# Optimization experiments

Measured on AMD Instinct MI355X. Metric: run time of the kernel, lower is better.

## Reference

```python
import jax, jax.numpy as jnp
import numpy as np
import math

B, D, L, Nh, Dk, Dv, K, CONV_NUM = 16, 256, 1024, 8, 32, 32, 7, 4
EPS = 1e-5


def _pos_encoding():
    # matches PosEncoder: freqs/phases per channel, sin(pos*freqs + phases), shape [D, L]
    idx = jnp.arange(D)
    i = idx.astype(jnp.float32)
    even = (idx % 2 == 0)
    freqs = jnp.where(even, 10000.0 ** (-i / D), -(10000.0 ** ((1.0 - i) / D)))
    phases = jnp.where(even, 0.0, math.pi / 2)
    pos = jnp.arange(L, dtype=jnp.float32)
    return jnp.sin(pos[None, :] * freqs[:, None] + phases[:, None])


def _layer_norm(x, g, b):
    # nn.LayerNorm([D, L]) on [B, D, L]: normalize over last two dims
    m = jnp.mean(x, axis=(1, 2), keepdims=True)
    v = jnp.mean((x - m) ** 2, axis=(1, 2), keepdims=True)
    return (x - m) * jax.lax.rsqrt(v + EPS) * g + b


def _ds_conv(x, dw, db, pw, pb):
    # depthwise conv1d (groups=D, same padding) + pointwise 1x1 conv
    y = jax.lax.conv_general_dilated(
        x, dw[:, None, :], window_strides=(1,), padding=[(K // 2, K // 2)],
        feature_group_count=D, dimension_numbers=('NCH', 'OIH', 'NCH'))
    y = y + db[None, :, None]
    return jnp.einsum('bdl,ed->bel', y, pw) + pb[None, :, None]


def setup_inputs() -> dict:
    key = jax.random.key(0)
    ks = jax.random.split(key, 12)

    def n(k, shape, scale):
        return jax.random.normal(k, shape, jnp.float32) * scale

    x = jax.random.normal(ks[0], (B, D, L), jnp.float32)
    mask = jax.random.randint(ks[1], (B, L), 0, 2).astype(jnp.int32)
    dw_w = n(ks[2], (CONV_NUM, D, K), 0.1)
    dw_b = jnp.zeros((CONV_NUM, D), jnp.float32)
    pw_w = n(ks[3], (CONV_NUM, D, D), 0.05)
    pw_b = jnp.zeros((CONV_NUM, D), jnp.float32)
    ln_g = jnp.ones((CONV_NUM + 2, D, L), jnp.float32)
    ln_b = jnp.zeros((CONV_NUM + 2, D, L), jnp.float32)
    Wq = n(ks[4], (Nh, D, Dk), 0.05)
    Wk = n(ks[5], (Nh, D, Dk), 0.05)
    Wv = n(ks[6], (Nh, D, Dv), 0.05)
    Wo = n(ks[7], (D, Dv * Nh), 0.05)
    fc_w = n(ks[8], (D, D), 0.05)
    fc_b = jnp.zeros((D,), jnp.float32)
    return dict(x=x, mask=mask, dw_w=dw_w, dw_b=dw_b, pw_w=pw_w, pw_b=pw_b,
                ln_g=ln_g, ln_b=ln_b, Wq=Wq, Wk=Wk, Wv=Wv, Wo=Wo,
                fc_w=fc_w, fc_b=fc_b)


def reference(x, mask, dw_w, dw_b, pw_w, pw_b, ln_g, ln_b, Wq, Wk, Wv, Wo, fc_w, fc_b):
    m = mask.astype(jnp.float32)  # [B, L]
    out = x + _pos_encoding()[None]
    res = out
    out = _layer_norm(out, ln_g[0], ln_b[0])
    for i in range(CONV_NUM):
        out = jax.nn.relu(_ds_conv(out, dw_w[i], dw_b[i], pw_w[i], pw_b[i])) + res
        # F.dropout in eval mode is identity
        res = out
        out = _layer_norm(out, ln_g[i + 1], ln_b[i + 1])
    # self attention (batched over heads instead of per-head loop; same math)
    xt = out.transpose(0, 2, 1)  # [B, L, D]
    q = jnp.einsum('bld,hdk->bhlk', xt, Wq)
    k = jnp.einsum('bld,hdk->bhlk', xt, Wk)
    v = jnp.einsum('bld,hdv->bhlv', xt, Wv)
    scores = jnp.einsum('bhqk,bhlk->bhql', q, k) * (1.0 / math.sqrt(Dk))
    hm = m[:, None, None, :]  # mask over key dim
    scores = scores * hm + (1.0 - hm) * (-1e30)
    attn = jax.nn.softmax(scores, axis=-1) * m[:, None, :, None]  # zero padded query rows
    heads = jnp.einsum('bhql,bhlv->bqhv', attn, v).reshape(B, L, Nh * Dv)  # head-major concat
    att_out = (heads @ Wo).transpose(0, 2, 1)  # [B, D, L]
    out = att_out + res
    res = out
    out = _layer_norm(out, ln_g[CONV_NUM + 1], ln_b[CONV_NUM + 1])
    out = jnp.einsum('bdl,ed->bel', out, fc_w) + fc_b[None, :, None]  # nn.Linear on [B,L,D]
    out = jax.nn.relu(out) + res
    return out
```

## Files before the change

### kernel.cpp

```cpp
#include <hip/hip_runtime.h>
#include <hip/hip_bf16.h>

#define NB 16
#define ND 256
#define NL 1024
#define NHH 8
#define NDK 32
#define NKW 7
#define NCONV 4
#define NPB (ND*NL)

constexpr float LN_EPS = 1e-5f;

typedef __attribute__((ext_vector_type(4))) float f32x4;
typedef __attribute__((ext_vector_type(4))) short bf16x4;
typedef __attribute__((ext_vector_type(8))) short bf16x8;

__device__ __forceinline__ short bf16s(float f){
  return (short)__builtin_bit_cast(unsigned short, __float2bfloat16(f));
}
__device__ __forceinline__ float b2f(short s){
  return __builtin_bit_cast(float, ((unsigned)(unsigned short)s) << 16);
}

__device__ __forceinline__ void ln_ab(const float* st, int slot, int b, float& mean, float& rstd){
  float s = 0.f, ss = 0.f;
  #pragma unroll
  for(int bin=0;bin<8;bin++){
    const float* p = st + ((size_t)((slot*NB+b)*8+bin))*32;
    s += p[0]; ss += p[1];
  }
  mean = s * (1.0f/NPB);
  float var = ss * (1.0f/NPB) - mean*mean;
  rstd = rsqrtf(var + LN_EPS);
}

__device__ __forceinline__ void stats_reduce(float s, float ss, float* stats, int slot, int b, int bin){
  __shared__ float red[8];
  #pragma unroll
  for(int o=32;o>0;o>>=1){ s += __shfl_down(s,o); ss += __shfl_down(ss,o); }
  int lane = threadIdx.x & 63, w = threadIdx.x >> 6;
  if(lane==0){ red[w*2]=s; red[w*2+1]=ss; }
  __syncthreads();
  if(threadIdx.x==0){
    float* p = stats + ((size_t)((slot*NB+b)*8+bin))*32;
    atomicAdd(&p[0], red[0]+red[2]+red[4]+red[6]);
    atomicAdd(&p[1], red[1]+red[3]+red[5]+red[7]);
  }
}

__global__ __launch_bounds__(256) void k_prep(const float* __restrict__ pw_w, const float* __restrict__ fc_w,
    const float* __restrict__ Wo, const float* __restrict__ Wq, const float* __restrict__ Wk,
    const float* __restrict__ Wv, const float* __restrict__ g, const float* __restrict__ btab,
    short* __restrict__ Wpwb, short* __restrict__ Wfcb, short* __restrict__ Wob, short* __restrict__ Wcat,
    short* __restrict__ gT, short* __restrict__ bT, float* __restrict__ postab){
  __shared__ float T[64][65];
  int blk = blockIdx.x, tid = threadIdx.x;
  if(blk < 256){
    int idx = blk*1024 + tid*4;
    f32x4 v = *(const f32x4*)(pw_w + idx);
    bf16x4 o;
    #pragma unroll
    for(int j=0;j<4;j++) o[j] = bf16s(v[j]);
    *(bf16x4*)(Wpwb + idx) = o;
  } else if(blk < 320){
    int idx = (blk-256)*1024 + tid*4;
    f32x4 v = *(const f32x4*)(fc_w + idx);
    bf16x4 o;
    #pragma unroll
    for(int j=0;j<4;j++) o[j] = bf16s(v[j]);
    *(bf16x4*)(Wfcb + idx) = o;
  } else if(blk < 384){
    int idx = (blk-320)*1024 + tid*4;
    int e = idx >> 8;
    bf16x4 o;
    #pragma unroll
    for(int j=0;j<4;j++){ int d = (idx+j)&255; o[j] = bf16s(Wo[d*ND + e]); }
    *(bf16x4*)(Wob + idx) = o;
  } else if(blk < 576){
    int idx = (blk-384)*1024 + tid*4;
    int og = idx >> 8, d = idx & 255;
    int seg = og >> 8, o = og & 255, h = o >> 5, k = o & 31;
    const float* W = (seg==0) ? Wq : ((seg==1) ? Wk : Wv);
    bf16x4 ov;
    #pragma unroll
    for(int j=0;j<4;j++) ov[j] = bf16s(W[((size_t)(h*ND + d + j))*NDK + k]);
    *(bf16x4*)(Wcat + idx) = ov;
  } else if(blk < 832){
    int d = blk - 576;
    int l = tid*4;
    const float LN1E4_OVER_D = 9.210340371976184f / (float)ND;
    float freq, phase;
    if((d & 1) == 0){ freq =  __expf(-(float)d*LN1E4_OVER_D);      phase = 0.f; }
    else            { freq = -__expf((1.f-(float)d)*LN1E4_OVER_D); phase = 1.5707963267948966f; }
    f32x4 o;
    #pragma unroll
    for(int j=0;j<4;j++) o[j] = sinf((float)(l+j)*freq + phase);
    *(f32x4*)(postab + ((size_t)d<<10) + l) = o;
  } else {
    int blk2 = blk - 832;
    int which = blk2 >> 6;
    int tile = blk2 & 63;
    int d0 = (tile & 3) << 6, l0 = (tile >> 2) << 6;
    const float* src = (which < 6) ? (g + (size_t)which*NPB) : (btab + (size_t)(which-6)*NPB);
    short* dst = (which < 6) ? (gT + (size_t)which*NPB) : (bT + (size_t)(which-6)*NPB);
    for(int i=tid;i<1024;i+=256){
      int dd = i>>4, l4 = i&15;
      f32x4 v = *(const f32x4*)(src + (size_t)(d0+dd)*NL + l0 + l4*4);
      #pragma unroll
      for(int j=0;j<4;j++) T[dd][l4*4+j] = v[j];
    }
    __syncthreads();
    for(int i=tid;i<1024;i+=256){
      int ll = i>>4, d4 = i&15;
      bf16x4 o;
      #pragma unroll
      for(int j=0;j<4;j++) o[j] = bf16s(T[d4*4+j][ll]);
      *(bf16x4*)(dst + (size_t)(l0+ll)*ND + d0 + d4*4) = o;
    }
  }
}

__global__ __launch_bounds__(256) void k_posadd(const float* __restrict__ x, const float* __restrict__ postab,
                                                float* __restrict__ R, float* __restrict__ stats){
  int blk = blockIdx.x;
  int lt = blk & 15, dt = (blk>>4)&3, b = blk>>6;
  int l0 = lt*64, d0 = dt*64;
  __shared__ float T[64][65];
  int tid = threadIdx.x;
  float s=0.f, ss=0.f;
  for(int i=tid;i<1024;i+=256){
    int dd = i>>4, l4 = i&15;
    int d = d0+dd;
    f32x4 xv = *(const f32x4*)(x + ((size_t)(b*ND+d)<<10) + l0 + l4*4);
    f32x4 pv = *(const f32x4*)(postab + ((size_t)d<<10) + l0 + l4*4);
    #pragma unroll
    for(int j=0;j<4;j++){
      float v = xv[j] + pv[j];
      T[dd][l4*4+j] = v;
      s += v; ss += v*v;
    }
  }
  __syncthreads();
  for(int i=tid;i<1024;i+=256){
    int ll = i>>4, d4 = i&15;
    f32x4 o;
    #pragma unroll
    for(int j=0;j<4;j++) o[j] = T[d4*4+j][ll];
    *(f32x4*)(R + ((size_t)(b*NL+l0+ll)<<8) + d0 + d4*4) = o;
  }
  stats_reduce(s, ss, stats, 0, b, blk & 7);
}

__global__ __launch_bounds__(256) void k_dwconvT(const float* __restrict__ R, const short* __restrict__ gT,
                                                 const short* __restrict__ bT, const float* __restrict__ w7,
                                                 const float* __restrict__ db, const float* __restrict__ stats,
                                                 short* __restrict__ Y, int slot){
  int blk = blockIdx.x;
  int lblk = blk & 63, b = blk >> 6;
  int tid = threadIdx.x;
  __shared__ float wLds[NKW][ND];
  __shared__ float dbLds[ND];
  for(int i=tid;i<ND*NKW;i+=256){ int d=i/NKW, q=i-d*NKW; wLds[q][d] = w7[i]; }
  dbLds[tid] = db[tid];
  float mean, rstd; ln_ab(stats, slot, b, mean, rstd);
  float mr = mean*rstd;
  __syncthreads();
  int d0 = (tid & 63)*4;
  int l0 = lblk*16 + (tid >> 6)*4;
  f32x4 ln[10];
  #pragma unroll
  for(int i=0;i<10;i++){
    int lp = l0 - 3 + i;
    if(lp >= 0 && lp < NL){
      f32x4 v = *(const f32x4*)(R + ((size_t)(b*NL+lp)<<8) + d0);
      bf16x4 gv = *(const bf16x4*)(gT + ((size_t)lp<<8) + d0);
      bf16x4 bv = *(const bf16x4*)(bT + ((size_t)lp<<8) + d0);
      f32x4 t;
      #pragma unroll
      for(int j=0;j<4;j++) t[j] = (v[j]*rstd - mr)*b2f(gv[j]) + b2f(bv[j]);
      ln[i] = t;
    } else ln[i] = (f32x4){0.f,0.f,0.f,0.f};
  }
  f32x4 dbv = *(const f32x4*)(&dbLds[d0]);
  #pragma unroll
  for(int jl=0;jl<4;jl++){
    f32x4 acc = dbv;
    #pragma unroll
    for(int q=0;q<NKW;q++){
      f32x4 wq = *(const f32x4*)(&wLds[q][d0]);
      #pragma unroll
      for(int j=0;j<4;j++) acc[j] += ln[jl+q][j]*wq[j];
    }
    bf16x4 o;
    #pragma unroll
    for(int j=0;j<4;j++) o[j] = bf16s(acc[j]);
    *(bf16x4*)(Y + ((size_t)(b*NL + l0 + jl)<<8) + d0) = o;
  }
}

__device__ __forceinline__ void stage_rows_bf16(short* dst, const short* src, int tid, int c){
  for(int i=tid;i<1024;i+=256){
    int rr = i>>4, kk = i&15;
    bf16x8 w = *(const bf16x8*)(src + (size_t)rr*ND + c*128 + kk*8);
    *(bf16x8*)((char*)dst + rr*256 + ((kk*16) ^ ((rr&7)<<4))) = w;
  }
}
__device__ __forceinline__ void stage_act_ln(short* dst, const float* src, const short* g, const short* bt,
                                             float mean, float rstd, int tid, int c){
  float mr = mean*rstd;
  for(int i=tid;i<2048;i+=256){
    int ll = i>>5, kk = i&31;
    size_t off = (size_t)ll*ND + c*128 + kk*4;
    f32x4 v = *(const f32x4*)(src + off);
    bf16x4 gv = *(const bf16x4*)(g + off);
    bf16x4 bv = *(const bf16x4*)(bt + off);
    bf16x4 o;
    #pragma unroll
    for(int j=0;j<4;j++) o[j] = bf16s((v[j]*rstd - mr)*b2f(gv[j]) + b2f(bv[j]));
    *(bf16x4*)((char*)dst + ll*256 + ((kk*8) ^ ((ll&7)<<4))) = o;
  }
}
__device__ __forceinline__ void mfma_core(const short* As, const short* Bs, int wm, int wn,
                                          int lq, int gg, f32x4 acc[2][2]){
  #pragma unroll
  for(int t=0;t<4;t++){
    bf16x8 a[2], bb[2];
    #pragma unroll
    for(int m=0;m<2;m++){
      int row = wm*32 + m*16 + lq;
      a[m] = *(const bf16x8*)((const char*)As + row*256 + ((t*64 + gg*16) ^ ((row&7)<<4)));
    }
    #pragma unroll
    for(int n=0;n<2;n++){
      int row = wn*32 + n*16 + lq;
      bb[n] = *(const bf16x8*)((const char*)Bs + row*256 + ((t*64 + gg*16) ^ ((row&7)<<4)));
    }
    #pragma unroll
    for(int m=0;m<2;m++)
      #pragma unroll
      for(int n=0;n<2;n++)
        acc[m][n] = __builtin_amdgcn_mfma_f32_16x16x32_bf16(a[m], bb[n], acc[m][n], 0,0,0);
  }
}

#define GEMM_PROLOGUE() \
  int blk = blockIdx.x; \
  int lt = blk & 15, et = (blk>>4)&3, b = blk>>6; \
  int l0 = lt*64, e0 = et*64; \
  int tid = threadIdx.x; \
  int w = tid>>6, lane = tid&63, lq = lane&15, gg = lane>>4; \
  int wm = w&1, wn = w>>1; \
  __shared__ short As[8192], Bs[8192]; \
  f32x4 acc[2][2]; \
  acc[0][0]=acc[0][1]=acc[1][0]=acc[1][1] = (f32x4){0.f,0.f,0.f,0.f};

__global__ __launch_bounds__(256) void k_pw(const short* __restrict__ Y, const short* __restrict__ Wb,
                                            const float* __restrict__ bias, float* __restrict__ R,
                                            float* __restrict__ stats, int slot_out){
  GEMM_PROLOGUE();
  const short* Asrc = Y + ((size_t)(b*NL)+l0)*ND;
  const short* Bsrc = Wb + (size_t)e0*ND;
  for(int c=0;c<2;c++){
    __syncthreads();
    stage_rows_bf16(As, Asrc, tid, c);
    stage_rows_bf16(Bs, Bsrc, tid, c);
    __syncthreads();
    mfma_core(As, Bs, wm, wn, lq, gg, acc);
  }
  float s=0.f, ss=0.f;
  #pragma unroll
  for(int n=0;n<2;n++){
    int e = e0 + wn*32 + n*16 + lq;
    float bv = bias[e];
    #pragma unroll
    for(int m=0;m<2;m++){
      #pragma unroll
      for(int r=0;r<4;r++){
        int l = l0 + wm*32 + m*16 + gg*4 + r;
        size_t ix = (size_t)(b*NL+l)*ND + e;
        float v = fmaxf(acc[m][n][r] + bv, 0.f);
        float rr = R[ix] + v;
        R[ix] = rr;
        s += rr; ss += rr*rr;
      }
    }
  }
  stats_reduce(s, ss, stats, slot_out, b, blk & 7);
}

__global__ __launch_bounds__(256) void k_qkvf(const float* __restrict__ R, const short* __restrict__ gT,
                                              const short* __restrict__ bT, const float* __restrict__ stats,
                                              const short* __restrict__ Wcat, short* __restrict__ Qb,
                                              short* __restrict__ Kb, short* __restrict__ Vb){
  int blk = blockIdx.x;
  int lt = blk & 15;
  int tmp = blk >> 4;
  int et = tmp % 12, b = tmp / 12;
  int l0 = lt*64, e0g = et*64;
  int seg = et >> 2;
  int tid = threadIdx.x;
  int w = tid>>6, lane = tid&63, lq = lane&15, gg = lane>>4;
  int wm = w&1, wn = w>>1;
  __shared__ short As[8192], Bs[8192];
  f32x4 acc[2][2];
  acc[0][0]=acc[0][1]=acc[1][0]=acc[1][1] = (f32x4){0.f,0.f,0.f,0.f};
  float mean, rstd; ln_ab(stats, 4, b, mean, rstd);
  const float* Asrc = R + ((size_t)(b*NL)+l0)*ND;
  const short* gs = gT + (size_t)l0*ND;
  const short* bs = bT + (size_t)l0*ND;
  const short* Bsrc = Wcat + (size_t)e0g*ND;
  for(int c=0;c<2;c++){
    __syncthreads();
    stage_act_ln(As, Asrc, gs, bs, mean, rstd, tid, c);
    stage_rows_bf16(Bs, Bsrc, tid, c);
    __syncthreads();
    mfma_core(As, Bs, wm, wn, lq, gg, acc);
  }
  #pragma unroll
  for(int n=0;n<2;n++){
    int eo = (et&3)*64 + wn*32 + n*16 + lq;
    int h = eo>>5, dk = eo&31;
    if(seg < 2){
      short* outp = (seg==0) ? Qb : Kb;
      #pragma unroll
      for(int m=0;m<2;m++){
        #pragma unroll
        for(int r=0;r<4;r++){
          int l = l0 + wm*32 + m*16 + gg*4 + r;
          outp[((size_t)(b*NHH+h)*NL + l)*NDK + dk] = bf16s(acc[m][n][r]);
        }
      }
    } else {
      #pragma unroll
      for(int m=0;m<2;m++){
        int lb = l0 + wm*32 + m*16 + gg*4;
        bf16x4 pk;
        #pragma unroll
        for(int r=0;r<4;r++) pk[r] = bf16s(acc[m][n][r]);
        *(bf16x4*)(Vb + ((size_t)(b*NHH+h)*NDK + dk)*NL + lb) = pk;
      }
    }
  }
}

__global__ __launch_bounds__(256) void k_attn(const short* __restrict__ Qb, const short* __restrict__ Kb,
                                              const short* __restrict__ Vt, const int* __restrict__ mask,
                                              short* __restrict__ heads){
  int blk = blockIdx.x;
  int qblk = blk & 15, h = (blk >> 4) & 7, b = blk >> 7;
  int bh = b*NHH + h;
  int tid = threadIdx.x;
  int w = tid >> 6, lane = tid & 63;
  int lq = lane & 15, gg = lane >> 4;

  __shared__ short Ks[64][40];
  __shared__ short Vs[32][72];
  __shared__ short Ps[4][16][40];
  __shared__ float msh[64];

  int qrow = qblk*64 + w*16 + lq;
  bf16x8 qf = *(const bf16x8*)(Qb + ((size_t)bh*NL + qrow)*NDK + gg*8);

  f32x4 zero = {0.f,0.f,0.f,0.f};
  f32x4 o0 = zero, o1 = zero;
  float dacc = 0.f;
  const float scale = 0.17677669529663687f;

  for(int t0=0; t0<NL; t0+=64){
    __syncthreads();
    {
      int key = tid >> 2, c = tid & 3;
      *(bf16x8*)(&Ks[key][c*8]) = *(const bf16x8*)(Kb + ((size_t)bh*NL + t0 + key)*NDK + c*8);
      int v = tid >> 3, ch = tid & 7;
      *(bf16x8*)(&Vs[v][ch*8]) = *(const bf16x8*)(Vt + ((size_t)bh*NDK + v)*NL + t0 + ch*8);
      if(tid < 64) msh[tid] = ((float)mask[b*NL + t0 + tid] - 1.f) * 1e30f;
    }
    __syncthreads();
    #pragma unroll
    for(int sub=0; sub<2; sub++){
      bf16x8 a0 = *(const bf16x8*)(&Ks[sub*32 + lq][gg*8]);
      bf16x8 a1 = *(const bf16x8*)(&Ks[sub*32 + 16 + lq][gg*8]);
      f32x4 c0 = __builtin_amdgcn_mfma_f32_16x16x32_bf16(a0, qf, zero, 0, 0, 0);
      f32x4 c1 = __builtin_amdgcn_mfma_f32_16x16x32_bf16(a1, qf, zero, 0, 0, 0);
      bf16x4 p0, p1;
      #pragma unroll
      for(int r=0;r<4;r++){
        float pv0 = __expf(__builtin_fmaf(c0[r], scale, msh[sub*32 + gg*4 + r]));
        dacc += pv0;
        p0[r] = bf16s(pv0);
        float pv1 = __expf(__builtin_fmaf(c1[r], scale, msh[sub*32 + 16 + gg*4 + r]));
        dacc += pv1;
        p1[r] = bf16s(pv1);
      }
      *(bf16x4*)(&Ps[w][lq][gg*4])      = p0;
      *(bf16x4*)(&Ps[w][lq][16 + gg*4]) = p1;
      bf16x8 pf = *(const bf16x8*)(&Ps[w][lq][gg*8]);
      bf16x8 b0 = *(const bf16x8*)(&Vs[lq][sub*32 + gg*8]);
      bf16x8 b1 = *(const bf16x8*)(&Vs[16 + lq][sub*32 + gg*8]);
      o0 = __builtin_amdgcn_mfma_f32_16x16x32_bf16(pf, b0, o0, 0, 0, 0);
      o1 = __builtin_amdgcn_mfma_f32_16x16x32_bf16(pf, b1, o1, 0, 0, 0);
    }
  }
  dacc += __shfl_xor(dacc, 16);
  dacc += __shfl_xor(dacc, 32);
  #pragma unroll
  for(int r=0;r<4;r++){
    int ql = gg*4 + r;
    float dn = __shfl(dacc, ql);
    int qg = qblk*64 + w*16 + ql;
    float mq = (float)mask[b*NL + qg];
    float sc = mq / dn;
    short* op = heads + ((size_t)(b*NL + qg))*(NHH*NDK) + h*NDK;
    op[lq]      = bf16s(o0[r]*sc);
    op[16 + lq] = bf16s(o1[r]*sc);
  }
}

__global__ __launch_bounds__(256) void k_wo(const short* __restrict__ H, const short* __restrict__ Wb,
                                            float* __restrict__ R, float* __restrict__ stats){
  GEMM_PROLOGUE();
  const short* Asrc = H + ((size_t)(b*NL)+l0)*ND;
  const short* Bsrc = Wb + (size_t)e0*ND;
  for(int c=0;c<2;c++){
    __syncthreads();
    stage_rows_bf16(As, Asrc, tid, c);
    stage_rows_bf16(Bs, Bsrc, tid, c);
    __syncthreads();
    mfma_core(As, Bs, wm, wn, lq, gg, acc);
  }
  float s=0.f, ss=0.f;
  #pragma unroll
  for(int n=0;n<2;n++){
    int e = e0 + wn*32 + n*16 + lq;
    #pragma unroll
    for(int m=0;m<2;m++){
      #pragma unroll
      for(int r=0;r<4;r++){
        int l = l0 + wm*32 + m*16 + gg*4 + r;
        size_t ix = (size_t)(b*NL+l)*ND + e;
        float rr = R[ix] + acc[m][n][r];
        R[ix] = rr;
        s += rr; ss += rr*rr;
      }
    }
  }
  stats_reduce(s, ss, stats, 5, b, blk & 7);
}

__global__ __launch_bounds__(256) void k_fc(const float* __restrict__ R, const short* __restrict__ gT,
                                            const short* __restrict__ bT, const float* __restrict__ stats,
                                            const short* __restrict__ Wb, const float* __restrict__ bias,
                                            float* __restrict__ out){
  GEMM_PROLOGUE();
  float mean, rstd; ln_ab(stats, 5, b, mean, rstd);
  const float* Asrc = R + ((size_t)(b*NL)+l0)*ND;
  const short* gs = gT + (size_t)l0*ND;
  const short* bs = bT + (size_t)l0*ND;
  const short* Bsrc = Wb + (size_t)e0*ND;
  for(int c=0;c<2;c++){
    __syncthreads();
    stage_act_ln(As, Asrc, gs, bs, mean, rstd, tid, c);
    stage_rows_bf16(Bs, Bsrc, tid, c);
    __syncthreads();
    mfma_core(As, Bs, wm, wn, lq, gg, acc);
  }
  #pragma unroll
  for(int n=0;n<2;n++){
    int e = e0 + wn*32 + n*16 + lq;
    float bv = bias[e];
    #pragma unroll
    for(int m=0;m<2;m++){
      int lb = l0 + wm*32 + m*16 + gg*4;
      f32x4 ov;
      #pragma unroll
      for(int r=0;r<4;r++){
        float v = fmaxf(acc[m][n][r] + bv, 0.f);
        ov[r] = v + R[(size_t)(b*NL+lb+r)*ND + e];
      }
      *(f32x4*)(out + (size_t)(b*ND+e)*NL + lb) = ov;
    }
  }
}

extern "C" void kernel_launch(void* const* d_in, const int* in_sizes, int n_in,
                              void* d_out, int out_size, void* d_ws, size_t ws_size,
                              hipStream_t stream){
  const float* x    = (const float*)d_in[0];
  const int*   mask = (const int*)d_in[1];
  const float* dw_w = (const float*)d_in[2];
  const float* dw_b = (const float*)d_in[3];
  const float* pw_w = (const float*)d_in[4];
  const float* pw_b = (const float*)d_in[5];
  const float* ln_g = (const float*)d_in[6];
  const float* ln_b = (const float*)d_in[7];
  const float* Wq   = (const float*)d_in[8];
  const float* Wk   = (const float*)d_in[9];
  const float* Wv   = (const float*)d_in[10];
  const float* Wo   = (const float*)d_in[11];
  const float* fc_w = (const float*)d_in[12];
  const float* fc_b = (const float*)d_in[13];

  float* ws     = (float*)d_ws;
  float* stats  = ws;
  float* postab = ws + 98304;
  float* R      = ws + 360448;
  short* Yb     = (short*)(ws + 4554752);
  short* Qb     = (short*)(ws + 6651904);
  short* Kb     = (short*)(ws + 8749056);
  short* Vb     = (short*)(ws + 10846208);
  short* gT     = (short*)(ws + 12943360);
  short* bT     = (short*)(ws + 13729792);
  short* Wpwb   = (short*)(ws + 14516224);
  short* Wfcb   = (short*)(ws + 14647296);
  short* Wob    = (short*)(ws + 14680064);
  short* Wcat   = (short*)(ws + 14712832);

  hipMemsetAsync(stats, 0, 98304*sizeof(float), stream);
  k_prep<<<1600,256,0,stream>>>(pw_w, fc_w, Wo, Wq, Wk, Wv, ln_g, ln_b,
                                Wpwb, Wfcb, Wob, Wcat, gT, bT, postab);
  k_posadd<<<1024,256,0,stream>>>(x, postab, R, stats);
  for(int i=0;i<NCONV;i++){
    k_dwconvT<<<1024,256,0,stream>>>(R, gT + (size_t)i*NPB, bT + (size_t)i*NPB,
                                     dw_w + i*ND*NKW, dw_b + i*ND, stats, Yb, i);
    k_pw<<<1024,256,0,stream>>>(Yb, Wpwb + (size_t)i*65536, pw_b + i*ND, R, stats, i+1);
  }
  k_qkvf<<<3072,256,0,stream>>>(R, gT + (size_t)4*NPB, bT + (size_t)4*NPB, stats, Wcat, Qb, Kb, Vb);
  k_attn<<<2048,256,0,stream>>>(Qb, Kb, Vb, mask, Yb);
  k_wo<<<1024,256,0,stream>>>(Yb, Wob, R, stats);
  k_fc<<<1024,256,0,stream>>>(R, gT + (size_t)5*NPB, bT + (size_t)5*NPB, stats, Wfcb, fc_b, (float*)d_out);
}
```

Measured before the change: 313.2 us.

## Store residual stream in bf16 and compute attention row sums via MFMA

Converts the residual buffer R from fp32 to bf16 across all kernels, roughly halving the bytes read and written for the residual in the posadd, dwconv, pw, qkv, wo and fc stages. LayerNorm statistics are now computed from the rounded bf16 values. The attention kernel also swaps the scalar softmax-denominator accumulation and its shuffles for an extra MFMA against a ones vector, and reorders block indexing so q-blocks of the same head are spread across the grid. The main risk is accuracy: the residual accumulates bf16 rounding over six layers.

```diff
diff --git a/kernel.cpp b/kernel.cpp
--- a/kernel.cpp
+++ b/kernel.cpp
@@ -122,37 +122,38 @@
 }
 
 __global__ __launch_bounds__(256) void k_posadd(const float* __restrict__ x, const float* __restrict__ postab,
-                                                float* __restrict__ R, float* __restrict__ stats){
+                                                short* __restrict__ Rb, float* __restrict__ stats){
   int blk = blockIdx.x;
   int lt = blk & 15, dt = (blk>>4)&3, b = blk>>6;
   int l0 = lt*64, d0 = dt*64;
   __shared__ float T[64][65];
   int tid = threadIdx.x;
-  float s=0.f, ss=0.f;
   for(int i=tid;i<1024;i+=256){
     int dd = i>>4, l4 = i&15;
     int d = d0+dd;
     f32x4 xv = *(const f32x4*)(x + ((size_t)(b*ND+d)<<10) + l0 + l4*4);
     f32x4 pv = *(const f32x4*)(postab + ((size_t)d<<10) + l0 + l4*4);
     #pragma unroll
-    for(int j=0;j<4;j++){
-      float v = xv[j] + pv[j];
-      T[dd][l4*4+j] = v;
-      s += v; ss += v*v;
-    }
+    for(int j=0;j<4;j++) T[dd][l4*4+j] = xv[j] + pv[j];
   }
   __syncthreads();
+  float s=0.f, ss=0.f;
   for(int i=tid;i<1024;i+=256){
     int ll = i>>4, d4 = i&15;
-    f32x4 o;
-    #pragma unroll
-    for(int j=0;j<4;j++) o[j] = T[d4*4+j][ll];
-    *(f32x4*)(R + ((size_t)(b*NL+l0+ll)<<8) + d0 + d4*4) = o;
+    bf16x4 o;
+    #pragma unroll
+    for(int j=0;j<4;j++){
+      short rs = bf16s(T[d4*4+j][ll]);
+      o[j] = rs;
+      float rv = b2f(rs);
+      s += rv; ss += rv*rv;
+    }
+    *(bf16x4*)(Rb + ((size_t)(b*NL+l0+ll)<<8) + d0 + d4*4) = o;
   }
   stats_reduce(s, ss, stats, 0, b, blk & 7);
 }
 
-__global__ __launch_bounds__(256) void k_dwconvT(const float* __restrict__ R, const short* __restrict__ gT,
+__global__ __launch_bounds__(256) void k_dwconvT(const short* __restrict__ Rb, const short* __restrict__ gT,
                                                  const short* __restrict__ bT, const float* __restrict__ w7,
                                                  const float* __restrict__ db, const float* __restrict__ stats,
                                                  short* __restrict__ Y, int slot){
@@ -173,12 +174,12 @@
   for(int i=0;i<10;i++){
     int lp = l0 - 3 + i;
     if(lp >= 0 && lp < NL){
-      f32x4 v = *(const f32x4*)(R + ((size_t)(b*NL+lp)<<8) + d0);
+      bf16x4 v = *(const bf16x4*)(Rb + ((size_t)(b*NL+lp)<<8) + d0);
       bf16x4 gv = *(const bf16x4*)(gT + ((size_t)lp<<8) + d0);
       bf16x4 bv = *(const bf16x4*)(bT + ((size_t)lp<<8) + d0);
       f32x4 t;
       #pragma unroll
-      for(int j=0;j<4;j++) t[j] = (v[j]*rstd - mr)*b2f(gv[j]) + b2f(bv[j]);
+      for(int j=0;j<4;j++) t[j] = (b2f(v[j])*rstd - mr)*b2f(gv[j]) + b2f(bv[j]);
       ln[i] = t;
     } else ln[i] = (f32x4){0.f,0.f,0.f,0.f};
   }
@@ -206,19 +207,19 @@
     *(bf16x8*)((char*)dst + rr*256 + ((kk*16) ^ ((rr&7)<<4))) = w;
   }
 }
-__device__ __forceinline__ void stage_act_ln(short* dst, const float* src, const short* g, const short* bt,
-                                             float mean, float rstd, int tid, int c){
+__device__ __forceinline__ void stage_act_lnb(short* dst, const short* src, const short* g, const short* bt,
+                                              float mean, float rstd, int tid, int c){
   float mr = mean*rstd;
-  for(int i=tid;i<2048;i+=256){
-    int ll = i>>5, kk = i&31;
-    size_t off = (size_t)ll*ND + c*128 + kk*4;
-    f32x4 v = *(const f32x4*)(src + off);
-    bf16x4 gv = *(const bf16x4*)(g + off);
-    bf16x4 bv = *(const bf16x4*)(bt + off);
-    bf16x4 o;
-    #pragma unroll
-    for(int j=0;j<4;j++) o[j] = bf16s((v[j]*rstd - mr)*b2f(gv[j]) + b2f(bv[j]));
-    *(bf16x4*)((char*)dst + ll*256 + ((kk*8) ^ ((ll&7)<<4))) = o;
+  for(int i=tid;i<1024;i+=256){
+    int ll = i>>4, kk = i&15;
+    size_t off = (size_t)ll*ND + c*128 + kk*8;
+    bf16x8 v = *(const bf16x8*)(src + off);
+    bf16x8 gv = *(const bf16x8*)(g + off);
+    bf16x8 bv = *(const bf16x8*)(bt + off);
+    bf16x8 o;
+    #pragma unroll
+    for(int j=0;j<8;j++) o[j] = bf16s((b2f(v[j])*rstd - mr)*b2f(gv[j]) + b2f(bv[j]));
+    *(bf16x8*)((char*)dst + ll*256 + ((kk*16) ^ ((ll&7)<<4))) = o;
   }
 }
 __device__ __forceinline__ void mfma_core(const short* As, const short* Bs, int wm, int wn,
@@ -256,7 +257,7 @@
   acc[0][0]=acc[0][1]=acc[1][0]=acc[1][1] = (f32x4){0.f,0.f,0.f,0.f};
 
 __global__ __launch_bounds__(256) void k_pw(const short* __restrict__ Y, const short* __restrict__ Wb,
-                                            const float* __restrict__ bias, float* __restrict__ R,
+                                            const float* __restrict__ bias, short* __restrict__ Rb,
                                             float* __restrict__ stats, int slot_out){
   GEMM_PROLOGUE();
   const short* Asrc = Y + ((size_t)(b*NL)+l0)*ND;
@@ -280,16 +281,18 @@
         int l = l0 + wm*32 + m*16 + gg*4 + r;
         size_t ix = (size_t)(b*NL+l)*ND + e;
         float v = fmaxf(acc[m][n][r] + bv, 0.f);
-        float rr = R[ix] + v;
-        R[ix] = rr;
-        s += rr; ss += rr*rr;
+        float rr = b2f(Rb[ix]) + v;
+        short rs = bf16s(rr);
+        Rb[ix] = rs;
+        float r2 = b2f(rs);
+        s += r2; ss += r2*r2;
       }
     }
   }
   stats_reduce(s, ss, stats, slot_out, b, blk & 7);
 }
 
-__global__ __launch_bounds__(256) void k_qkvf(const float* __restrict__ R, const short* __restrict__ gT,
+__global__ __launch_bounds__(256) void k_qkvf(const short* __restrict__ Rb, const short* __restrict__ gT,
                                               const short* __restrict__ bT, const float* __restrict__ stats,
                                               const short* __restrict__ Wcat, short* __restrict__ Qb,
                                               short* __restrict__ Kb, short* __restrict__ Vb){
@@ -306,13 +309,13 @@
   f32x4 acc[2][2];
   acc[0][0]=acc[0][1]=acc[1][0]=acc[1][1] = (f32x4){0.f,0.f,0.f,0.f};
   float mean, rstd; ln_ab(stats, 4, b, mean, rstd);
-  const float* Asrc = R + ((size_t)(b*NL)+l0)*ND;
+  const short* Asrc = Rb + ((size_t)(b*NL)+l0)*ND;
   const short* gs = gT + (size_t)l0*ND;
   const short* bs = bT + (size_t)l0*ND;
   const short* Bsrc = Wcat + (size_t)e0g*ND;
   for(int c=0;c<2;c++){
     __syncthreads();
-    stage_act_ln(As, Asrc, gs, bs, mean, rstd, tid, c);
+    stage_act_lnb(As, Asrc, gs, bs, mean, rstd, tid, c);
     stage_rows_bf16(Bs, Bsrc, tid, c);
     __syncthreads();
     mfma_core(As, Bs, wm, wn, lq, gg, acc);
@@ -348,8 +351,8 @@
                                               const short* __restrict__ Vt, const int* __restrict__ mask,
                                               short* __restrict__ heads){
   int blk = blockIdx.x;
-  int qblk = blk & 15, h = (blk >> 4) & 7, b = blk >> 7;
-  int bh = b*NHH + h;
+  int qblk = blk >> 7, bh = blk & 127;
+  int b = bh >> 3, h = bh & 7;
   int tid = threadIdx.x;
   int w = tid >> 6, lane = tid & 63;
   int lq = lane & 15, gg = lane >> 4;
@@ -362,9 +365,12 @@
   int qrow = qblk*64 + w*16 + lq;
   bf16x8 qf = *(const bf16x8*)(Qb + ((size_t)bh*NL + qrow)*NDK + gg*8);
 
+  bf16x8 ones;
+  #pragma unroll
+  for(int j=0;j<8;j++) ones[j] = (short)0x3F80;
+
   f32x4 zero = {0.f,0.f,0.f,0.f};
-  f32x4 o0 = zero, o1 = zero;
-  float dacc = 0.f;
+  f32x4 o0 = zero, o1 = zero, o2 = zero;
   const float scale = 0.17677669529663687f;
 
   for(int t0=0; t0<NL; t0+=64){
@@ -387,10 +393,8 @@
       #pragma unroll
       for(int r=0;r<4;r++){
         float pv0 = __expf(__builtin_fmaf(c0[r], scale, msh[sub*32 + gg*4 + r]));
-        dacc += pv0;
         p0[r] = bf16s(pv0);
         float pv1 = __expf(__builtin_fmaf(c1[r], scale, msh[sub*32 + 16 + gg*4 + r]));
-        dacc += pv1;
         p1[r] = bf16s(pv1);
       }
       *(bf16x4*)(&Ps[w][lq][gg*4])      = p0;
@@ -400,17 +404,15 @@
       bf16x8 b1 = *(const bf16x8*)(&Vs[16 + lq][sub*32 + gg*8]);
       o0 = __builtin_amdgcn_mfma_f32_16x16x32_bf16(pf, b0, o0, 0, 0, 0);
       o1 = __builtin_amdgcn_mfma_f32_16x16x32_bf16(pf, b1, o1, 0, 0, 0);
-    }
-  }
-  dacc += __shfl_xor(dacc, 16);
-  dacc += __shfl_xor(dacc, 32);
+      o2 = __builtin_amdgcn_mfma_f32_16x16x32_bf16(pf, ones, o2, 0, 0, 0);
+    }
+  }
   #pragma unroll
   for(int r=0;r<4;r++){
     int ql = gg*4 + r;
-    float dn = __shfl(dacc, ql);
     int qg = qblk*64 + w*16 + ql;
     float mq = (float)mask[b*NL + qg];
-    float sc = mq / dn;
+    float sc = mq / o2[r];
     short* op = heads + ((size_t)(b*NL + qg))*(NHH*NDK) + h*NDK;
     op[lq]      = bf16s(o0[r]*sc);
     op[16 + lq] = bf16s(o1[r]*sc);
@@ -418,7 +420,7 @@
 }
 
 __global__ __launch_bounds__(256) void k_wo(const short* __restrict__ H, const short* __restrict__ Wb,
-                                            float* __restrict__ R, float* __restrict__ stats){
+                                            short* __restrict__ Rb, float* __restrict__ stats){
   GEMM_PROLOGUE();
   const short* Asrc = H + ((size_t)(b*NL)+l0)*ND;
   const short* Bsrc = Wb + (size_t)e0*ND;
@@ -439,28 +441,30 @@
       for(int r=0;r<4;r++){
         int l = l0 + wm*32 + m*16 + gg*4 + r;
         size_t ix = (size_t)(b*NL+l)*ND + e;
-        float rr = R[ix] + acc[m][n][r];
-        R[ix] = rr;
-        s += rr; ss += rr*rr;
+        float rr = b2f(Rb[ix]) + acc[m][n][r];
+        short rs = bf16s(rr);
+        Rb[ix] = rs;
+        float r2 = b2f(rs);
+        s += r2; ss += r2*r2;
       }
     }
   }
   stats_reduce(s, ss, stats, 5, b, blk & 7);
 }
 
-__global__ __launch_bounds__(256) void k_fc(const float* __restrict__ R, const short* __restrict__ gT,
+__global__ __launch_bounds__(256) void k_fc(const short* __restrict__ Rb, const short* __restrict__ gT,
                                             const short* __restrict__ bT, const float* __restrict__ stats,
                                             const short* __restrict__ Wb, const float* __restrict__ bias,
                                             float* __restrict__ out){
   GEMM_PROLOGUE();
   float mean, rstd; ln_ab(stats, 5, b, mean, rstd);
-  const float* Asrc = R + ((size_t)(b*NL)+l0)*ND;
+  const short* Asrc = Rb + ((size_t)(b*NL)+l0)*ND;
   const short* gs = gT + (size_t)l0*ND;
   const short* bs = bT + (size_t)l0*ND;
   const short* Bsrc = Wb + (size_t)e0*ND;
   for(int c=0;c<2;c++){
     __syncthreads();
-    stage_act_ln(As, Asrc, gs, bs, mean, rstd, tid, c);
+    stage_act_lnb(As, Asrc, gs, bs, mean, rstd, tid, c);
     stage_rows_bf16(Bs, Bsrc, tid, c);
     __syncthreads();
     mfma_core(As, Bs, wm, wn, lq, gg, acc);
@@ -476,7 +480,7 @@
       #pragma unroll
       for(int r=0;r<4;r++){
         float v = fmaxf(acc[m][n][r] + bv, 0.f);
-        ov[r] = v + R[(size_t)(b*NL+lb+r)*ND + e];
+        ov[r] = v + b2f(Rb[(size_t)(b*NL+lb+r)*ND + e]);
       }
       *(f32x4*)(out + (size_t)(b*ND+e)*NL + lb) = ov;
     }
@@ -504,29 +508,29 @@
   float* ws     = (float*)d_ws;
   float* stats  = ws;
   float* postab = ws + 98304;
-  float* R      = ws + 360448;
-  short* Yb     = (short*)(ws + 4554752);
-  short* Qb     = (short*)(ws + 6651904);
-  short* Kb     = (short*)(ws + 8749056);
-  short* Vb     = (short*)(ws + 10846208);
-  short* gT     = (short*)(ws + 12943360);
-  short* bT     = (short*)(ws + 13729792);
-  short* Wpwb   = (short*)(ws + 14516224);
-  short* Wfcb   = (short*)(ws + 14647296);
-  short* Wob    = (short*)(ws + 14680064);
-  short* Wcat   = (short*)(ws + 14712832);
+  short* Rb     = (short*)(ws + 360448);
+  short* Yb     = (short*)(ws + 2457600);
+  short* Qb     = (short*)(ws + 4554752);
+  short* Kb     = (short*)(ws + 6651904);
+  short* Vb     = (short*)(ws + 8749056);
+  short* gT     = (short*)(ws + 10846208);
+  short* bT     = (short*)(ws + 11632640);
+  short* Wpwb   = (short*)(ws + 12419072);
+  short* Wfcb   = (short*)(ws + 12550144);
+  short* Wob    = (short*)(ws + 12582912);
+  short* Wcat   = (short*)(ws + 12615680);
 
   hipMemsetAsync(stats, 0, 98304*sizeof(float), stream);
   k_prep<<<1600,256,0,stream>>>(pw_w, fc_w, Wo, Wq, Wk, Wv, ln_g, ln_b,
                                 Wpwb, Wfcb, Wob, Wcat, gT, bT, postab);
-  k_posadd<<<1024,256,0,stream>>>(x, postab, R, stats);
+  k_posadd<<<1024,256,0,stream>>>(x, postab, Rb, stats);
   for(int i=0;i<NCONV;i++){
-    k_dwconvT<<<1024,256,0,stream>>>(R, gT + (size_t)i*NPB, bT + (size_t)i*NPB,
+    k_dwconvT<<<1024,256,0,stream>>>(Rb, gT + (size_t)i*NPB, bT + (size_t)i*NPB,
                                      dw_w + i*ND*NKW, dw_b + i*ND, stats, Yb, i);
-    k_pw<<<1024,256,0,stream>>>(Yb, Wpwb + (size_t)i*65536, pw_b + i*ND, R, stats, i+1);
-  }
-  k_qkvf<<<3072,256,0,stream>>>(R, gT + (size_t)4*NPB, bT + (size_t)4*NPB, stats, Wcat, Qb, Kb, Vb);
+    k_pw<<<1024,256,0,stream>>>(Yb, Wpwb + (size_t)i*65536, pw_b + i*ND, Rb, stats, i+1);
+  }
+  k_qkvf<<<3072,256,0,stream>>>(Rb, gT + (size_t)4*NPB, bT + (size_t)4*NPB, stats, Wcat, Qb, Kb, Vb);
   k_attn<<<2048,256,0,stream>>>(Qb, Kb, Vb, mask, Yb);
-  k_wo<<<1024,256,0,stream>>>(Yb, Wob, R, stats);
-  k_fc<<<1024,256,0,stream>>>(R, gT + (size_t)5*NPB, bT + (size_t)5*NPB, stats, Wfcb, fc_b, (float*)d_out);
-}
+  k_wo<<<1024,256,0,stream>>>(Yb, Wob, Rb, stats);
+  k_fc<<<1024,256,0,stream>>>(Rb, gT + (size_t)5*NPB, bT + (size_t)5*NPB, stats, Wfcb, fc_b, (float*)d_out);
+}
```

After: 304.7 us. 1.03x faster.
